# Performance work log

Measured on AMD Instinct MI355X. Metric: run time of the kernel, lower is better.

The kernel has to match this reference:

```python
import jax, jax.numpy as jnp
import numpy as np

CH = 128
GROUPS = 8
EPS = 1e-5

def group_norm(x, w, b):
    B, C, H, W = x.shape
    g = x.reshape(B, GROUPS, C // GROUPS, H, W)
    mean = g.mean(axis=(2, 3, 4), keepdims=True)
    var = g.var(axis=(2, 3, 4), keepdims=True)
    g = (g - mean) * jax.lax.rsqrt(var + EPS)
    g = g.reshape(B, C, H, W)
    return g * w[None, :, None, None] + b[None, :, None, None]

def setup_inputs() -> dict:
    key = jax.random.key(0)
    ks = jax.random.split(key, 7)
    C = CH
    x = jax.random.normal(ks[0], (8, C, 64, 64), dtype=jnp.float32)
    gn_w = jnp.ones((C,), dtype=jnp.float32)
    gn_b = jnp.zeros((C,), dtype=jnp.float32)
    s = 1.0 / np.sqrt(C)
    qkv_w = jax.random.normal(ks[1], (3 * C, C), dtype=jnp.float32) * s
    qkv_b = jax.random.normal(ks[2], (3 * C,), dtype=jnp.float32) * 0.01
    proj_w = jax.random.normal(ks[3], (C, C), dtype=jnp.float32) * s
    proj_b = jax.random.normal(ks[4], (C,), dtype=jnp.float32) * 0.01
    return {"x": x, "gn_w": gn_w, "gn_b": gn_b, "qkv_w": qkv_w,
            "qkv_b": qkv_b, "proj_w": proj_w, "proj_b": proj_b}

def reference(x, gn_w, gn_b, qkv_w, qkv_b, proj_w, proj_b):
    B, C, H, W = x.shape
    h = group_norm(x, gn_w, gn_b)
    # 1x1 conv == per-pixel matmul over channels
    qkv = jnp.einsum('bchw,oc->bohw', h, qkv_w) + qkv_b[None, :, None, None]
    q, k, v = jnp.split(qkv.reshape(B, 3 * C, H * W), 3, axis=1)  # each [B,C,N]
    scale = C ** (-0.5)
    attn = jax.nn.softmax(jnp.einsum('bci,bcj->bij', q * scale, k), axis=-1)
    out = jnp.einsum('bij,bcj->bci', attn, v).reshape(B, C, H, W)
    out = jnp.einsum('bchw,oc->bohw', out, proj_w) + proj_b[None, :, None, None]
    return x + out
```

## Files before the change

### kernel.cpp

```cpp
#include <hip/hip_runtime.h>
#include <stdint.h>


typedef __attribute__((ext_vector_type(8))) short short8;
typedef __attribute__((ext_vector_type(4))) float f32x4;
typedef __attribute__((ext_vector_type(16))) float f32x16;

#define MFMA_BF16(a, b, c) __builtin_amdgcn_mfma_f32_16x16x32_bf16((a), (b), (c), 0, 0, 0)
#define MFMA32(a, b, c) __builtin_amdgcn_mfma_f32_32x32x16_bf16((a), (b), (c), 0, 0, 0)
#define EXP2(x) __builtin_amdgcn_exp2f(x)

#define QSCALE 0.12751743f

__device__ __forceinline__ unsigned short f2bf(float f) {
    unsigned int u = __builtin_bit_cast(unsigned int, f);
    u += 0x7FFFu + ((u >> 16) & 1u);
    return (unsigned short)(u >> 16);
}
__device__ __forceinline__ float bf2f(unsigned int lo16) {
    return __builtin_bit_cast(float, lo16 << 16);
}
__device__ __forceinline__ short8 ldg8(const unsigned short* p) {
    return __builtin_bit_cast(short8, *(const uint4*)p);
}
__device__ __forceinline__ unsigned int cvtpk(float lo, float hi) {
    unsigned int r;
    asm("v_cvt_pk_bf16_f32 %0, %1, %2" : "=v"(r) : "v"(lo), "v"(hi));
    return r;
}
__device__ __forceinline__ void gload16(const void* g, void* l) {
    __builtin_amdgcn_global_load_lds(
        (__attribute__((address_space(1))) void*)g,
        (__attribute__((address_space(3))) void*)l, 16, 0, 0);
}

__global__ __launch_bounds__(256) void k_pre(const float* __restrict__ x,
                                             float* __restrict__ sums,
                                             const float* __restrict__ qkv_w,
                                             const float* __restrict__ proj_w,
                                             unsigned short* __restrict__ wq,
                                             unsigned short* __restrict__ wp) {
    if (blockIdx.x >= 1024) {
        int i = ((blockIdx.x - 1024) * 256 + threadIdx.x) * 4;
        const float* src; unsigned short* dst; int off;
        if (i < 49152) { src = qkv_w; dst = wq; off = i; }
        else           { src = proj_w; dst = wp; off = i - 49152; }
        float4 v = *(const float4*)(src + off);
        uint2 pk;
        pk.x = (unsigned int)f2bf(v.x) | ((unsigned int)f2bf(v.y) << 16);
        pk.y = (unsigned int)f2bf(v.z) | ((unsigned int)f2bf(v.w) << 16);
        *(uint2*)(dst + off) = pk;
        return;
    }
    int g     = blockIdx.x >> 4;
    int slice = blockIdx.x & 15;
    const float* p = x + (size_t)g * 65536 + slice * 4096;
    float s = 0.f, sq = 0.f;
#pragma unroll
    for (int i = 0; i < 4; ++i) {
        float4 v = *(const float4*)(p + threadIdx.x * 4 + i * 1024);
        s  += v.x + v.y + v.z + v.w;
        sq += v.x*v.x + v.y*v.y + v.z*v.z + v.w*v.w;
    }
#pragma unroll
    for (int m = 1; m < 64; m <<= 1) { s += __shfl_xor(s, m, 64); sq += __shfl_xor(sq, m, 64); }
    __shared__ float ss[4], ssq[4];
    int w = threadIdx.x >> 6;
    if ((threadIdx.x & 63) == 0) { ss[w] = s; ssq[w] = sq; }
    __syncthreads();
    if (threadIdx.x == 0) {
        sums[(g * 16 + slice) * 2]     = ss[0] + ss[1] + ss[2] + ss[3];
        sums[(g * 16 + slice) * 2 + 1] = ssq[0] + ssq[1] + ssq[2] + ssq[3];
    }
}

__global__ __launch_bounds__(256) void k_qkv(const float* __restrict__ x,
                                             const float* __restrict__ sums,
                                             const float* __restrict__ gn_w,
                                             const float* __restrict__ gn_b,
                                             const unsigned short* __restrict__ wq,
                                             const float* __restrict__ qkv_b,
                                             unsigned short* __restrict__ q_ws,
                                             unsigned short* __restrict__ k_ws,
                                             unsigned short* __restrict__ v_ws) {
    __shared__ unsigned short h_lds[64][144];
    __shared__ float ms[8][2];
    const int tid  = threadIdx.x;
    const int b    = blockIdx.x >> 6;
    const int n0   = (blockIdx.x & 63) << 6;
    const int lane = tid & 63, wave = tid >> 6;
    const int l15  = lane & 15, q4 = lane >> 4;

    if (tid < 8) {
        float s = 0.f, q = 0.f;
        const float* sp = sums + (size_t)(b * 8 + tid) * 32;
#pragma unroll
        for (int i = 0; i < 16; ++i) { s += sp[i * 2]; q += sp[i * 2 + 1]; }
        float mean = s * (1.f / 65536.f);
        float var  = q * (1.f / 65536.f) - mean * mean;
        ms[tid][0] = mean;
        ms[tid][1] = rsqrtf(var + 1e-5f);
    }
    __syncthreads();

    {
        int cb = tid >> 4;
        int nn = (tid & 15) << 2;
#pragma unroll
        for (int k = 0; k < 8; ++k) {
            int c = cb + (k << 4);
            float4 v = *(const float4*)(x + ((size_t)(b * 128 + c) << 12) + n0 + nn);
            int g = c >> 4;
            float mean = ms[g][0];
            float rstd = ms[g][1];
            float ga = gn_w[c] * rstd;
            float be = gn_b[c] - mean * ga;
            h_lds[nn + 0][c] = f2bf(v.x * ga + be);
            h_lds[nn + 1][c] = f2bf(v.y * ga + be);
            h_lds[nn + 2][c] = f2bf(v.z * ga + be);
            h_lds[nn + 3][c] = f2bf(v.w * ga + be);
        }
    }
    __syncthreads();

    short8 bfrag[4][4];
#pragma unroll
    for (int nt = 0; nt < 4; ++nt)
#pragma unroll
        for (int ks = 0; ks < 4; ++ks)
            bfrag[nt][ks] = *(const short8*)&h_lds[nt * 16 + l15][ks * 32 + q4 * 8];
    __syncthreads();

    unsigned short* vstage = &h_lds[0][0];

#pragma unroll
    for (int ot = 0; ot < 6; ++ot) {
        int o0 = wave * 96 + ot * 16;
        short8 af[4];
#pragma unroll
        for (int ks = 0; ks < 4; ++ks)
            af[ks] = ldg8(wq + (size_t)(o0 + l15) * 128 + ks * 32 + q4 * 8);

        if (o0 < 256) {
            float bias[4];
#pragma unroll
            for (int r = 0; r < 4; ++r) bias[r] = qkv_b[o0 + q4 * 4 + r];
            float qs = (o0 < 128) ? QSCALE : 1.0f;
#pragma unroll
            for (int nt = 0; nt < 4; ++nt) {
                f32x4 acc = {0.f, 0.f, 0.f, 0.f};
#pragma unroll
                for (int ks = 0; ks < 4; ++ks)
                    acc = MFMA_BF16(af[ks], bfrag[nt][ks], acc);
                int n = n0 + nt * 16 + l15;
                unsigned short* dst = (o0 < 128) ? q_ws : k_ws;
                int oo = (o0 < 128) ? o0 : (o0 - 128);
                unsigned int lo = (unsigned int)f2bf((acc[0] + bias[0]) * qs) |
                                  ((unsigned int)f2bf((acc[1] + bias[1]) * qs) << 16);
                unsigned int hi = (unsigned int)f2bf((acc[2] + bias[2]) * qs) |
                                  ((unsigned int)f2bf((acc[3] + bias[3]) * qs) << 16);
                uint2 pk; pk.x = lo; pk.y = hi;
                *(uint2*)&dst[((size_t)(b * 4096 + n) << 7) + oo + q4 * 4] = pk;
            }
        } else {
            int c = o0 - 256 + l15;
            float vb = qkv_b[o0 + l15];
#pragma unroll
            for (int nt = 0; nt < 4; ++nt) {
                f32x4 acc = {0.f, 0.f, 0.f, 0.f};
#pragma unroll
                for (int ks = 0; ks < 4; ++ks)
                    acc = MFMA_BF16(bfrag[nt][ks], af[ks], acc);
                unsigned int lo = (unsigned int)f2bf(acc[0] + vb) |
                                  ((unsigned int)f2bf(acc[1] + vb) << 16);
                unsigned int hi = (unsigned int)f2bf(acc[2] + vb) |
                                  ((unsigned int)f2bf(acc[3] + vb) << 16);
                uint2 pk; pk.x = lo; pk.y = hi;
                *(uint2*)&vstage[c * 72 + nt * 16 + q4 * 4] = pk;
            }
        }
    }
    __syncthreads();

    {
        int c = tid >> 1, hf = tid & 1;
        const unsigned short* src = vstage + c * 72 + hf * 32;
        unsigned short* dst = v_ws + ((size_t)(b * 128 + c) << 12) + n0 + hf * 32;
        uint4 a0 = *(const uint4*)(src + 0);
        uint4 a1 = *(const uint4*)(src + 8);
        uint4 a2 = *(const uint4*)(src + 16);
        uint4 a3 = *(const uint4*)(src + 24);
        *(uint4*)(dst + 0)  = a0;
        *(uint4*)(dst + 8)  = a1;
        *(uint4*)(dst + 16) = a2;
        *(uint4*)(dst + 24) = a3;
    }
}

__global__ __launch_bounds__(512, 2) void k_attn(const unsigned short* __restrict__ q_ws,
                                                 const unsigned short* __restrict__ k_ws,
                                                 const unsigned short* __restrict__ v_ws,
                                                 const float* __restrict__ x,
                                                 const unsigned short* __restrict__ wp,
                                                 const float* __restrict__ proj_b,
                                                 float* __restrict__ out) {
    __shared__ unsigned short K0[64][128];
    __shared__ unsigned short K1[64][128];
    __shared__ unsigned short V0[128][64];
    __shared__ unsigned short V1[128][64];
    __shared__ unsigned short O_lds[128][136];
    __shared__ float Lp[256];

    const int tid   = threadIdx.x;
    const int b     = blockIdx.x & 7;
    const int tile  = blockIdx.x >> 3;
    const int i0    = tile << 7;
    const int lane  = tid & 63, wave = tid >> 6;
    const int ih    = wave >> 1, jh = wave & 1;
    const int l31   = lane & 31, h = lane >> 5;

    short8 qf[8];
    {
        const unsigned short* qp =
            q_ws + ((size_t)(b * 4096 + i0 + ih * 32 + l31) << 7) + h * 8;
#pragma unroll
        for (int ks = 0; ks < 8; ++ks) qf[ks] = ldg8(qp + ks * 16);
    }

    f32x16 acc[4];
#pragma unroll
    for (int ct = 0; ct < 4; ++ct)
#pragma unroll
        for (int e = 0; e < 16; ++e) acc[ct][e] = 0.f;
    float l_run = 0.f;

    const unsigned short* kbase = k_ws + ((size_t)b << 19);
    int ksrc[2];
#pragma unroll
    for (int q = 0; q < 2; ++q) {
        int c   = q * 512 + tid;
        int row = c >> 4;
        ksrc[q] = row * 16 + ((c & 15) ^ (row & 15));
    }
    const unsigned short* vlane = v_ws + ((size_t)b << 19) +
        ((size_t)(tid >> 3) << 12) +
        ((((tid & 7) ^ ((tid >> 3) & 7) ^ wave)) << 3);

#define STAGE(T, KD, VD)                                                              \
  do {                                                                                \
    _Pragma("unroll")                                                                 \
    for (int q = 0; q < 2; ++q)                                                       \
      gload16(kbase + (size_t)(T) * 8192 + ksrc[q] * 8,                               \
              (char*)(&KD[0][0]) + q * 8192 + wave * 1024);                           \
    _Pragma("unroll")                                                                 \
    for (int q = 0; q < 2; ++q)                                                       \
      gload16(vlane + (size_t)q * 262144 + (T) * 64,                                  \
              (char*)(&VD[0][0]) + q * 8192 + wave * 1024);                           \
  } while (0)

#define BAR_A()                                                                       \
  do {                                                                                \
    asm volatile("s_waitcnt vmcnt(0)" ::: "memory");                                  \
    __builtin_amdgcn_s_barrier();                                                     \
    __builtin_amdgcn_sched_barrier(0);                                                \
  } while (0)

    const int krow = jh * 32 + l31;
    const int ksw  = l31 & 15;
    const int vk   = (l31 & 7) ^ (l31 >> 3);
    const int irow = ih * 32 + l31;

    STAGE(0, K0, V0);

#define ATTN_ITER(IT, KR, VR, KP, VP)                                                 \
  do {                                                                                \
    BAR_A();                          \
    if ((IT) < 63) STAGE((IT) + 1, KP, VP);           \
    f32x16 s;        \
    _Pragma("unroll")                                                                 \
    for (int e = 0; e < 16; ++e) s[e] = 0.f;                                          \
    _Pragma("unroll")                                                                 \
    for (int ks = 0; ks < 8; ++ks) {                                                  \
      short8 kf = *(const short8*)&KR[krow][((ks * 2 + h) ^ ksw) << 3];               \
      s = MFMA32(kf, qf[ks], s);                                                      \
    }                                                                                 \
    float pvv[16];                         \
    _Pragma("unroll")                                                                 \
    for (int e = 0; e < 16; ++e) pvv[e] = EXP2(fminf(s[e], 30.f));                    \
    l_run += (((pvv[0] + pvv[1]) + (pvv[2] + pvv[3])) +                               \
              ((pvv[4] + pvv[5]) + (pvv[6] + pvv[7]))) +                              \
             (((pvv[8] + pvv[9]) + (pvv[10] + pvv[11])) +                             \
              ((pvv[12] + pvv[13]) + (pvv[14] + pvv[15])));                           \
    short8 paf[2];     \
    _Pragma("unroll")                                                                 \
    for (int ks = 0; ks < 2; ++ks) {                                                  \
      const float* pp = pvv + ks * 8;                                                 \
      unsigned int Wa = cvtpk(pp[0], pp[1]);                                          \
      unsigned int Wc = cvtpk(pp[2], pp[3]);                                          \
      unsigned int Wb = cvtpk(pp[4], pp[5]);                                          \
      unsigned int Wd = cvtpk(pp[6], pp[7]);                                          \
      auto r1 = __builtin_amdgcn_permlane32_swap(Wa, Wb, false, false);               \
      auto r2 = __builtin_amdgcn_permlane32_swap(Wc, Wd, false, false);               \
      uint4 aw; aw.x = r1[0]; aw.y = r2[0]; aw.z = r1[1]; aw.w = r2[1];               \
      paf[ks] = __builtin_bit_cast(short8, aw);              \
    }                                                                                 \
    _Pragma("unroll")                                                                 \
    for (int ks = 0; ks < 2; ++ks)                                                    \
      _Pragma("unroll")                                                               \
      for (int ct = 0; ct < 4; ++ct) {                                                \
        short8 vf = *(const short8*)&VR[ct * 32 + l31]                                \
            [((jh * 4 + ks * 2 + h) ^ vk ^ ((ct & 1) << 2)) << 3];                    \
        acc[ct] = MFMA32(paf[ks], vf, acc[ct]);                                       \
      }                                                                               \
  } while (0)

    for (int ib = 0; ib < 32; ++ib) {
        int it = ib * 2;
        ATTN_ITER(it,     K0, V0, K1, V1);
        ATTN_ITER(it + 1, K1, V1, K0, V0);
    }
#undef ATTN_ITER
#undef STAGE
#undef BAR_A

    __syncthreads();
    float l2 = l_run + __shfl_xor(l_run, 32);
    if (h == 0) Lp[jh * 128 + irow] = l2;
    float* ObLow  = (ih < 2) ? (float*)&K0[0][0] : (float*)&K1[0][0];
    float* ObHigh = (ih < 2) ? (float*)&V0[0][0] : (float*)&V1[0][0];
    const int vbase = (ih & 1) * 32;
    if (jh) {
#pragma unroll
        for (int cc = 0; cc < 2; ++cc)
#pragma unroll
            for (int r = 0; r < 16; ++r) {
                int il = (r & 3) + ((r >> 2) << 3) + (h << 2);
                ObLow[(vbase + il) * 64 + cc * 32 + l31] = (cc == 0) ? acc[0][r] : acc[1][r];
            }
    } else {
#pragma unroll
        for (int cc = 0; cc < 2; ++cc)
#pragma unroll
            for (int r = 0; r < 16; ++r) {
                int il = (r & 3) + ((r >> 2) << 3) + (h << 2);
                ObHigh[(vbase + il) * 64 + cc * 32 + l31] = (cc == 0) ? acc[2][r] : acc[3][r];
            }
    }
    __syncthreads();
    {
        float rl[16];
#pragma unroll
        for (int r = 0; r < 16; ++r) {
            int il = (r & 3) + ((r >> 2) << 3) + (h << 2);
            rl[r] = 1.0f / (Lp[ih * 32 + il] + Lp[128 + ih * 32 + il]);
        }
        if (jh) {
#pragma unroll
            for (int cc = 0; cc < 2; ++cc)
#pragma unroll
                for (int r = 0; r < 16; ++r) {
                    int il = (r & 3) + ((r >> 2) << 3) + (h << 2);
                    float own = (cc == 0) ? acc[2][r] : acc[3][r];
                    float v = own + ObHigh[(vbase + il) * 64 + cc * 32 + l31];
                    O_lds[ih * 32 + il][64 + cc * 32 + l31] = f2bf(v * rl[r]);
                }
        } else {
#pragma unroll
            for (int cc = 0; cc < 2; ++cc)
#pragma unroll
                for (int r = 0; r < 16; ++r) {
                    int il = (r & 3) + ((r >> 2) << 3) + (h << 2);
                    float own = (cc == 0) ? acc[0][r] : acc[1][r];
                    float v = own + ObLow[(vbase + il) * 64 + cc * 32 + l31];
                    O_lds[ih * 32 + il][cc * 32 + l31] = f2bf(v * rl[r]);
                }
        }
    }
    __syncthreads();

    {
        const int l15 = lane & 15, q4 = lane >> 4;
        int o0 = wave * 16;
        short8 af[4];
#pragma unroll
        for (int ks = 0; ks < 4; ++ks)
            af[ks] = ldg8(wp + (size_t)(o0 + l15) * 128 + ks * 32 + q4 * 8);
        float pb[4];
#pragma unroll
        for (int r = 0; r < 4; ++r) pb[r] = proj_b[o0 + q4 * 4 + r];

#pragma unroll
        for (int nt = 0; nt < 8; ++nt) {
            f32x4 pacc = {0.f, 0.f, 0.f, 0.f};
#pragma unroll
            for (int ks = 0; ks < 4; ++ks) {
                short8 bf = *(const short8*)&O_lds[nt * 16 + l15][ks * 32 + q4 * 8];
                pacc = MFMA_BF16(af[ks], bf, pacc);
            }
#pragma unroll
            for (int r = 0; r < 4; ++r) {
                size_t idx = ((size_t)(b * 128 + o0 + q4 * 4 + r) << 12) +
                             i0 + nt * 16 + l15;
                out[idx] = x[idx] + pacc[r] + pb[r];
            }
        }
    }
}

extern "C" void kernel_launch(void* const* d_in, const int* in_sizes, int n_in,
                              void* d_out, int out_size, void* d_ws, size_t ws_size,
                              hipStream_t stream) {
    const float* x      = (const float*)d_in[0];
    const float* gn_w   = (const float*)d_in[1];
    const float* gn_b   = (const float*)d_in[2];
    const float* qkv_w  = (const float*)d_in[3];
    const float* qkv_b  = (const float*)d_in[4];
    const float* proj_w = (const float*)d_in[5];
    const float* proj_b = (const float*)d_in[6];
    float* out = (float*)d_out;

    char* ws = (char*)d_ws;
    float* sums           = (float*)ws;
    unsigned short* wq    = (unsigned short*)(ws + 16384);
    unsigned short* wp    = (unsigned short*)(ws + 16384 + 98304);
    unsigned short* q_ws  = (unsigned short*)(ws + ((size_t)1  << 20));
    unsigned short* k_ws  = (unsigned short*)(ws + ((size_t)9  << 20));
    unsigned short* v_ws  = (unsigned short*)(ws + ((size_t)17 << 20));

    k_pre<<<1088, 256, 0, stream>>>(x, sums, qkv_w, proj_w, wq, wp);
    k_qkv<<<512, 256, 0, stream>>>(x, sums, gn_w, gn_b, wq, qkv_b, q_ws, k_ws, v_ws);
    k_attn<<<256, 512, 0, stream>>>(q_ws, k_ws, v_ws, x, wp, proj_b, out);
}
```

Measured before the change: 178.0 us.

## Fuse Q projection into attention kernel, dropping Q workspace round-trip

New measurement: 175.4 us. About the same (-1.5%).

```diff
diff --git a/kernel.cpp b/kernel.cpp
--- a/kernel.cpp
+++ b/kernel.cpp
@@ -80,7 +80,6 @@
                                              const float* __restrict__ gn_b,
                                              const unsigned short* __restrict__ wq,
                                              const float* __restrict__ qkv_b,
-                                             unsigned short* __restrict__ q_ws,
                                              unsigned short* __restrict__ k_ws,
                                              unsigned short* __restrict__ v_ws) {
     __shared__ unsigned short h_lds[64][144];
@@ -134,18 +133,17 @@
     unsigned short* vstage = &h_lds[0][0];
 
 #pragma unroll
-    for (int ot = 0; ot < 6; ++ot) {
-        int o0 = wave * 96 + ot * 16;
+    for (int ot = 0; ot < 4; ++ot) {
+        int o0 = wave * 64 + ot * 16;
         short8 af[4];
 #pragma unroll
         for (int ks = 0; ks < 4; ++ks)
-            af[ks] = ldg8(wq + (size_t)(o0 + l15) * 128 + ks * 32 + q4 * 8);
-
-        if (o0 < 256) {
+            af[ks] = ldg8(wq + (size_t)(128 + o0 + l15) * 128 + ks * 32 + q4 * 8);
+
+        if (o0 < 128) {
             float bias[4];
 #pragma unroll
-            for (int r = 0; r < 4; ++r) bias[r] = qkv_b[o0 + q4 * 4 + r];
-            float qs = (o0 < 128) ? QSCALE : 1.0f;
+            for (int r = 0; r < 4; ++r) bias[r] = qkv_b[128 + o0 + q4 * 4 + r];
 #pragma unroll
             for (int nt = 0; nt < 4; ++nt) {
                 f32x4 acc = {0.f, 0.f, 0.f, 0.f};
@@ -153,18 +151,16 @@
                 for (int ks = 0; ks < 4; ++ks)
                     acc = MFMA_BF16(af[ks], bfrag[nt][ks], acc);
                 int n = n0 + nt * 16 + l15;
-                unsigned short* dst = (o0 < 128) ? q_ws : k_ws;
-                int oo = (o0 < 128) ? o0 : (o0 - 128);
-                unsigned int lo = (unsigned int)f2bf((acc[0] + bias[0]) * qs) |
-                                  ((unsigned int)f2bf((acc[1] + bias[1]) * qs) << 16);
-                unsigned int hi = (unsigned int)f2bf((acc[2] + bias[2]) * qs) |
-                                  ((unsigned int)f2bf((acc[3] + bias[3]) * qs) << 16);
+                unsigned int lo = (unsigned int)f2bf(acc[0] + bias[0]) |
+                                  ((unsigned int)f2bf(acc[1] + bias[1]) << 16);
+                unsigned int hi = (unsigned int)f2bf(acc[2] + bias[2]) |
+                                  ((unsigned int)f2bf(acc[3] + bias[3]) << 16);
                 uint2 pk; pk.x = lo; pk.y = hi;
-                *(uint2*)&dst[((size_t)(b * 4096 + n) << 7) + oo + q4 * 4] = pk;
+                *(uint2*)&k_ws[((size_t)(b * 4096 + n) << 7) + o0 + q4 * 4] = pk;
             }
         } else {
-            int c = o0 - 256 + l15;
-            float vb = qkv_b[o0 + l15];
+            int c = o0 - 128 + l15;
+            float vb = qkv_b[128 + o0 + l15];
 #pragma unroll
             for (int nt = 0; nt < 4; ++nt) {
                 f32x4 acc = {0.f, 0.f, 0.f, 0.f};
@@ -197,7 +193,11 @@
     }
 }
 
-__global__ __launch_bounds__(512, 2) void k_attn(const unsigned short* __restrict__ q_ws,
+__global__ __launch_bounds__(512, 2) void k_attn(const float* __restrict__ sums,
+                                                 const float* __restrict__ gn_w,
+                                                 const float* __restrict__ gn_b,
+                                                 const unsigned short* __restrict__ wq,
+                                                 const float* __restrict__ qkv_b,
                                                  const unsigned short* __restrict__ k_ws,
                                                  const unsigned short* __restrict__ v_ws,
                                                  const float* __restrict__ x,
@@ -210,6 +210,7 @@
     __shared__ unsigned short V1[128][64];
     __shared__ unsigned short O_lds[128][136];
     __shared__ float Lp[256];
+    __shared__ float ms[8][2];
 
     const int tid   = threadIdx.x;
     const int b     = blockIdx.x & 7;
@@ -218,14 +219,76 @@
     const int lane  = tid & 63, wave = tid >> 6;
     const int ih    = wave >> 1, jh = wave & 1;
     const int l31   = lane & 31, h = lane >> 5;
+    const int irow  = ih * 32 + l31;
+
+    if (tid < 8) {
+        float s = 0.f, q = 0.f;
+        const float* sp = sums + (size_t)(b * 8 + tid) * 32;
+#pragma unroll
+        for (int i = 0; i < 16; ++i) { s += sp[i * 2]; q += sp[i * 2 + 1]; }
+        float mean = s * (1.f / 65536.f);
+        float var  = q * (1.f / 65536.f) - mean * mean;
+        ms[tid][0] = mean;
+        ms[tid][1] = rsqrtf(var + 1e-5f);
+    }
+    __syncthreads();
+
+    {
+        int c = tid >> 2, qq = tid & 3;
+        float mean = ms[c >> 4][0], rstd = ms[c >> 4][1];
+        float ga = gn_w[c] * rstd;
+        float be = gn_b[c] - mean * ga;
+        const float* xp = x + ((size_t)(b * 128 + c) << 12) + i0 + qq * 32;
+#pragma unroll
+        for (int k = 0; k < 8; ++k) {
+            float4 v = *(const float4*)(xp + k * 4);
+            int il = qq * 32 + k * 4;
+            O_lds[il + 0][c] = f2bf(v.x * ga + be);
+            O_lds[il + 1][c] = f2bf(v.y * ga + be);
+            O_lds[il + 2][c] = f2bf(v.z * ga + be);
+            O_lds[il + 3][c] = f2bf(v.w * ga + be);
+        }
+    }
+    __syncthreads();
+
+    {
+        const int l15 = lane & 15, q4 = lane >> 4;
+        int o0q = wave * 16;
+        short8 af[4];
+#pragma unroll
+        for (int ks = 0; ks < 4; ++ks)
+            af[ks] = ldg8(wq + (size_t)(o0q + l15) * 128 + ks * 32 + q4 * 8);
+        float qb[4];
+#pragma unroll
+        for (int r = 0; r < 4; ++r) qb[r] = qkv_b[o0q + q4 * 4 + r];
+#pragma unroll
+        for (int nt = 0; nt < 8; ++nt) {
+            f32x4 qacc = {0.f, 0.f, 0.f, 0.f};
+#pragma unroll
+            for (int ks = 0; ks < 4; ++ks) {
+                short8 bf = *(const short8*)&O_lds[nt * 16 + l15][ks * 32 + q4 * 8];
+                qacc = MFMA_BF16(af[ks], bf, qacc);
+            }
+            unsigned int lo = (unsigned int)f2bf((qacc[0] + qb[0]) * QSCALE) |
+                              ((unsigned int)f2bf((qacc[1] + qb[1]) * QSCALE) << 16);
+            unsigned int hi = (unsigned int)f2bf((qacc[2] + qb[2]) * QSCALE) |
+                              ((unsigned int)f2bf((qacc[3] + qb[3]) * QSCALE) << 16);
+            uint2 pk; pk.x = lo; pk.y = hi;
+            unsigned short* qrow = (nt < 4) ? &K0[nt * 16 + l15][0]
+                                            : &K1[(nt - 4) * 16 + l15][0];
+            *(uint2*)(qrow + o0q + q4 * 4) = pk;
+        }
+    }
+    __syncthreads();
 
     short8 qf[8];
     {
-        const unsigned short* qp =
-            q_ws + ((size_t)(b * 4096 + i0 + ih * 32 + l31) << 7) + h * 8;
-#pragma unroll
-        for (int ks = 0; ks < 8; ++ks) qf[ks] = ldg8(qp + ks * 16);
-    }
+        const unsigned short* qrow = (ih < 2) ? &K0[irow][0] : &K1[irow - 64][0];
+#pragma unroll
+        for (int ks = 0; ks < 8; ++ks)
+            qf[ks] = *(const short8*)(qrow + ks * 16 + h * 8);
+    }
+    __syncthreads();
 
     f32x16 acc[4];
 #pragma unroll
@@ -268,7 +331,6 @@
     const int krow = jh * 32 + l31;
     const int ksw  = l31 & 15;
     const int vk   = (l31 & 7) ^ (l31 >> 3);
-    const int irow = ih * 32 + l31;
 
     STAGE(0, K0, V0);
 
@@ -423,11 +485,11 @@
     float* sums           = (float*)ws;
     unsigned short* wq    = (unsigned short*)(ws + 16384);
     unsigned short* wp    = (unsigned short*)(ws + 16384 + 98304);
-    unsigned short* q_ws  = (unsigned short*)(ws + ((size_t)1  << 20));
-    unsigned short* k_ws  = (unsigned short*)(ws + ((size_t)9  << 20));
-    unsigned short* v_ws  = (unsigned short*)(ws + ((size_t)17 << 20));
+    unsigned short* k_ws  = (unsigned short*)(ws + ((size_t)1 << 20));
+    unsigned short* v_ws  = (unsigned short*)(ws + ((size_t)9 << 20));
 
     k_pre<<<1088, 256, 0, stream>>>(x, sums, qkv_w, proj_w, wq, wp);
-    k_qkv<<<512, 256, 0, stream>>>(x, sums, gn_w, gn_b, wq, qkv_b, q_ws, k_ws, v_ws);
-    k_attn<<<256, 512, 0, stream>>>(q_ws, k_ws, v_ws, x, wp, proj_b, out);
-}
+    k_qkv<<<512, 256, 0, stream>>>(x, sums, gn_w, gn_b, wq, qkv_b, k_ws, v_ws);
+    k_attn<<<256, 512, 0, stream>>>(sums, gn_w, gn_b, wq, qkv_b, k_ws, v_ws,
+                                    x, wp, proj_b, out);
+}
```
